# Performance work log

Measured on AMD Instinct MI355X. Metric: run time of the kernel, lower is better.

## Reference

```python
import jax, jax.numpy as jnp
import numpy as np

B, N, E, H = 8, 1024, 768, 12
HD = E // H

def setup_inputs() -> dict:
    key = jax.random.key(0)
    k1, k2, k3, k4, k5 = jax.random.split(key, 5)
    s = 0.02
    return {
        'query': jax.random.normal(k1, (B, N, E), dtype=jnp.float32),
        'qkv_w': jax.random.normal(k2, (3 * E, E), dtype=jnp.float32) * s,
        'qkv_b': jax.random.normal(k3, (3 * E,), dtype=jnp.float32) * s,
        'out_w': jax.random.normal(k4, (E, E), dtype=jnp.float32) * s,
        'out_b': jax.random.normal(k5, (E,), dtype=jnp.float32) * s,
    }

def reference(query, qkv_w, qkv_b, out_w, out_b):
    b, n, e = query.shape
    scale = HD ** -0.5
    # torch Linear: x @ W^T + b
    qkv = query @ qkv_w.T + qkv_b              # [B,N,3E]
    qkv = qkv.reshape(b, n, 3, H, HD)
    q = qkv[:, :, 0].transpose(0, 2, 1, 3)     # [B,H,N,hd]
    k = qkv[:, :, 1].transpose(0, 2, 1, 3)
    v = qkv[:, :, 2].transpose(0, 2, 1, 3)
    attn = jnp.einsum('bhqd,bhkd->bhqk', q, k) * scale
    attn = jax.nn.softmax(attn, axis=-1)
    x = jnp.einsum('bhqk,bhkd->bhqd', attn, v)  # [B,H,N,hd]
    x = x.transpose(0, 2, 1, 3).reshape(b, n, e)
    return x @ out_w.T + out_b
```

## Files before the change

### kernel.cpp

```cpp
#include <hip/hip_runtime.h>
#include <cstdint>
#include <cstddef>

#define QSCALE 0.18033688011112042f

typedef __bf16 bf16x8 __attribute__((ext_vector_type(8)));
typedef __bf16 bf16x4 __attribute__((ext_vector_type(4)));
typedef short short4v __attribute__((ext_vector_type(4)));
typedef float floatx4 __attribute__((ext_vector_type(4)));

static __device__ __forceinline__ uint16_t f2bf(float f) {
    uint32_t u = __builtin_bit_cast(uint32_t, f);
    u += 0x7FFFu + ((u >> 16) & 1u);
    return (uint16_t)(u >> 16);
}

static __device__ __forceinline__ void st_bf16(uint16_t* p, float f) {
    *(__bf16*)p = (__bf16)f;
}

static __device__ __forceinline__ bf16x8 ld_frag(const uint16_t* p) {
    uint4 u = *(const uint4*)p;
    return __builtin_bit_cast(bf16x8, u);
}

static __device__ __forceinline__ void async_lds16(const uint16_t* g, uint16_t* l) {
    __builtin_amdgcn_global_load_lds(
        (const __attribute__((address_space(1))) void*)g,
        (__attribute__((address_space(3))) void*)l,
        16, 0, 0);
}

static __device__ __forceinline__ size_t qk_swz(int bh, int idx, int hd) {
    return (size_t)bh * 65536 + (size_t)(idx >> 4) * 1024 + (size_t)(hd >> 5) * 512
         + (size_t)((hd & 31) >> 3) * 128 + (size_t)(idx & 15) * 8 + (hd & 7);
}
static __device__ __forceinline__ size_t v_swz(int bh, int hd, int key) {
    return (size_t)bh * 65536 + (size_t)(key >> 6) * 4096 + (size_t)(hd >> 4) * 1024
         + (size_t)((key >> 4) & 3) * 256 + (size_t)((key >> 2) & 3) * 64
         + (size_t)(hd & 15) * 4 + (key & 3);
}

__global__ __launch_bounds__(256) void cast3_kernel(
    const float* __restrict__ a, uint16_t* __restrict__ da, int na8,
    const float* __restrict__ b, uint16_t* __restrict__ db, int nb8,
    const float* __restrict__ c, uint16_t* __restrict__ dc, int nc8)
{
    int i = blockIdx.x * 256 + threadIdx.x;
    const float* src; uint16_t* dst; int idx;
    if (i < na8)                { src = a; dst = da; idx = i; }
    else if (i < na8 + nb8)     { src = b; dst = db; idx = i - na8; }
    else if (i < na8 + nb8 + nc8){ src = c; dst = dc; idx = i - na8 - nb8; }
    else return;
    const float4* p = (const float4*)src + (size_t)2 * idx;
    float4 x = p[0], y = p[1];
    uint32_t w0 = (uint32_t)f2bf(x.x) | ((uint32_t)f2bf(x.y) << 16);
    uint32_t w1 = (uint32_t)f2bf(x.z) | ((uint32_t)f2bf(x.w) << 16);
    uint32_t w2 = (uint32_t)f2bf(y.x) | ((uint32_t)f2bf(y.y) << 16);
    uint32_t w3 = (uint32_t)f2bf(y.z) | ((uint32_t)f2bf(y.w) << 16);
    uint4 v; v.x = w0; v.y = w1; v.z = w2; v.w = w3;
    *((uint4*)dst + idx) = v;
}

__global__ __launch_bounds__(256) void gemm_qkv_kernel(
    const uint16_t* __restrict__ X,
    const uint16_t* __restrict__ W,
    const float* __restrict__ bias,
    uint16_t* __restrict__ Qs, uint16_t* __restrict__ Ks, uint16_t* __restrict__ Vs)
{
    __shared__ __align__(16) uint16_t As[128 * 32];
    __shared__ __align__(16) uint16_t Bs[128 * 32];
    const int tid = threadIdx.x;
    const int wave = tid >> 6, lane = tid & 63;
    const int L = lane & 15, quad = lane >> 4;
    const int wM = (wave >> 1) * 64, wN = (wave & 1) * 64;
    const int bm = blockIdx.x * 128;
    const int bn = blockIdx.y * 128;

    floatx4 zero4 = {0.f, 0.f, 0.f, 0.f};
    floatx4 acc[4][4];
    #pragma unroll
    for (int i = 0; i < 4; ++i)
        #pragma unroll
        for (int j = 0; j < 4; ++j) acc[i][j] = zero4;

    const int srow = tid >> 2;
    const int scol = ((tid & 3) ^ ((srow >> 1) & 3)) * 8;
    const uint16_t* xp0 = X + (size_t)(bm + srow) * 768 + scol;
    const uint16_t* xp1 = xp0 + (size_t)64 * 768;
    const uint16_t* wp0 = W + (size_t)(bn + srow) * 768 + scol;
    const uint16_t* wp1 = wp0 + (size_t)64 * 768;
    uint16_t* lA0 = As + wave * 512;
    uint16_t* lA1 = As + 2048 + wave * 512;
    uint16_t* lB0 = Bs + wave * 512;
    uint16_t* lB1 = Bs + 2048 + wave * 512;

    const int cq = (quad ^ ((L >> 1) & 3)) * 8;

    for (int k0 = 0; k0 < 768; k0 += 32) {
        __syncthreads();
        async_lds16(xp0 + k0, lA0);
        async_lds16(xp1 + k0, lA1);
        async_lds16(wp0 + k0, lB0);
        async_lds16(wp1 + k0, lB1);
        __syncthreads();
        bf16x8 af[4], bfr[4];
        #pragma unroll
        for (int mi = 0; mi < 4; ++mi) af[mi]  = ld_frag(&As[(wM + mi * 16 + L) * 32 + cq]);
        #pragma unroll
        for (int ni = 0; ni < 4; ++ni) bfr[ni] = ld_frag(&Bs[(wN + ni * 16 + L) * 32 + cq]);
        #pragma unroll
        for (int mi = 0; mi < 4; ++mi)
            #pragma unroll
            for (int ni = 0; ni < 4; ++ni)
                acc[mi][ni] = __builtin_amdgcn_mfma_f32_16x16x32_bf16(
                    af[mi], bfr[ni], acc[mi][ni], 0, 0, 0);
    }

    const int part = bn / 768;
    #pragma unroll
    for (int ni = 0; ni < 4; ++ni) {
        int col = bn + wN + ni * 16 + L;
        int c = col - part * 768;
        int h = c >> 6, hd = c & 63;
        float bv = bias[col];
        #pragma unroll
        for (int mi = 0; mi < 4; ++mi) {
            #pragma unroll
            for (int r = 0; r < 4; ++r) {
                int m = bm + wM + mi * 16 + quad * 4 + r;
                int b = m >> 10, ns = m & 1023;
                int bh = b * 12 + h;
                float v = acc[mi][ni][r] + bv;
                if (part == 0)      st_bf16(&Qs[qk_swz(bh, ns, hd)], v * QSCALE);
                else if (part == 1) st_bf16(&Ks[qk_swz(bh, ns, hd)], v);
                else                st_bf16(&Vs[v_swz(bh, hd, ns)], v);
            }
        }
    }
}

__global__ __launch_bounds__(256) void attn_kernel(
    const uint16_t* __restrict__ Qs,
    const uint16_t* __restrict__ Ks,
    const uint16_t* __restrict__ Vs,
    uint16_t* __restrict__ Ob)
{
    const int tid = threadIdx.x;
    const int wave = tid >> 6, lane = tid & 63;
    const int L = lane & 15, quad = lane >> 4;
    const int bh = blockIdx.x;
    const int qt = blockIdx.y;
    const int b = bh / 12, h = bh - b * 12;
    const int q0 = qt * 128 + wave * 32;

    floatx4 zero4 = {0.f, 0.f, 0.f, 0.f};

    const uint16_t* qbase = Qs + (size_t)bh * 65536 + (size_t)lane * 8;
    bf16x8 aq[2][2];
    #pragma unroll
    for (int st = 0; st < 2; ++st) {
        const uint16_t* qp = qbase + (size_t)(qt * 8 + wave * 2 + st) * 1024;
        aq[st][0] = ld_frag(qp);
        aq[st][1] = ld_frag(qp + 512);
    }

    floatx4 accO[2][4];
    #pragma unroll
    for (int st = 0; st < 2; ++st)
        #pragma unroll
        for (int t = 0; t < 4; ++t) accO[st][t] = zero4;
    float lacc[2] = {0.f, 0.f};

    const uint16_t* kbase = Ks + (size_t)bh * 65536 + (size_t)lane * 8;
    const uint16_t* vbase = Vs + (size_t)bh * 65536 + (size_t)lane * 4;

    for (int j = 0; j < 16; ++j) {
        bf16x8 ka[4][2];
        #pragma unroll
        for (int kc = 0; kc < 4; ++kc) {
            const uint16_t* kp = kbase + (size_t)(j * 4 + kc) * 1024;
            ka[kc][0] = ld_frag(kp);
            ka[kc][1] = ld_frag(kp + 512);
        }
        short4v va[4][4];
        const uint16_t* vp = vbase + (size_t)j * 4096;
        #pragma unroll
        for (int t = 0; t < 4; ++t)
            #pragma unroll
            for (int kc = 0; kc < 4; ++kc)
                va[kc][t] = *(const short4v*)(vp + t * 1024 + kc * 256);

        floatx4 c[2][4];
        #pragma unroll
        for (int st = 0; st < 2; ++st)
            #pragma unroll
            for (int kc = 0; kc < 4; ++kc) {
                floatx4 z = zero4;
                z = __builtin_amdgcn_mfma_f32_16x16x32_bf16(ka[kc][0], aq[st][0], z, 0, 0, 0);
                z = __builtin_amdgcn_mfma_f32_16x16x32_bf16(ka[kc][1], aq[st][1], z, 0, 0, 0);
                c[st][kc] = z;
            }

        short4v pb[2][4];
        #pragma unroll
        for (int st = 0; st < 2; ++st)
            #pragma unroll
            for (int kc = 0; kc < 4; ++kc) {
                float p0 = __builtin_amdgcn_exp2f(c[st][kc][0]);
                float p1 = __builtin_amdgcn_exp2f(c[st][kc][1]);
                float p2 = __builtin_amdgcn_exp2f(c[st][kc][2]);
                float p3 = __builtin_amdgcn_exp2f(c[st][kc][3]);
                lacc[st] += (p0 + p1) + (p2 + p3);
                bf16x4 t4;
                t4.x = (__bf16)p0; t4.y = (__bf16)p1;
                t4.z = (__bf16)p2; t4.w = (__bf16)p3;
                pb[st][kc] = __builtin_bit_cast(short4v, t4);
            }

        #pragma unroll
        for (int st = 0; st < 2; ++st)
            #pragma unroll
            for (int t = 0; t < 4; ++t)
                #pragma unroll
                for (int kc = 0; kc < 4; ++kc)
                    accO[st][t] = __builtin_amdgcn_mfma_f32_16x16x16bf16_1k(
                        va[kc][t], pb[st][kc], accO[st][t], 0, 0, 0);
    }

    #pragma unroll
    for (int st = 0; st < 2; ++st) {
        float sum = lacc[st];
        sum += __shfl_xor(sum, 16);
        sum += __shfl_xor(sum, 32);
        float inv = 1.f / sum;
        uint16_t* orow = Ob + ((size_t)b * 1024 + q0 + st * 16 + L) * 768 + h * 64 + quad * 4;
        #pragma unroll
        for (int t = 0; t < 4; ++t) {
            bf16x4 o4;
            o4.x = (__bf16)(accO[st][t][0] * inv);
            o4.y = (__bf16)(accO[st][t][1] * inv);
            o4.z = (__bf16)(accO[st][t][2] * inv);
            o4.w = (__bf16)(accO[st][t][3] * inv);
            *(uint2*)(orow + t * 16) = __builtin_bit_cast(uint2, o4);
        }
    }
}

__global__ __launch_bounds__(256) void gemm_out_kernel(
    const uint16_t* __restrict__ X,
    const uint16_t* __restrict__ W,
    const float* __restrict__ bias,
    float* __restrict__ out)
{
    __shared__ __align__(16) uint16_t As[128 * 32];
    __shared__ __align__(16) uint16_t Bs[64 * 32];
    const int tid = threadIdx.x;
    const int wave = tid >> 6, lane = tid & 63;
    const int L = lane & 15, quad = lane >> 4;
    const int wM = (wave >> 1) * 64, wN = (wave & 1) * 32;
    const int bm = blockIdx.x * 128;
    const int bn = blockIdx.y * 64;

    floatx4 zero4 = {0.f, 0.f, 0.f, 0.f};
    floatx4 acc[4][2];
    #pragma unroll
    for (int i = 0; i < 4; ++i)
        #pragma unroll
        for (int j = 0; j < 2; ++j) acc[i][j] = zero4;

    const int srow = tid >> 2;
    const int scol = ((tid & 3) ^ ((srow >> 1) & 3)) * 8;
    const uint16_t* xp0 = X + (size_t)(bm + srow) * 768 + scol;
    const uint16_t* xp1 = xp0 + (size_t)64 * 768;
    const uint16_t* wp0 = W + (size_t)(bn + srow) * 768 + scol;
    uint16_t* lA0 = As + wave * 512;
    uint16_t* lA1 = As + 2048 + wave * 512;
    uint16_t* lB0 = Bs + wave * 512;

    const int cq = (quad ^ ((L >> 1) & 3)) * 8;

    for (int k0 = 0; k0 < 768; k0 += 32) {
        __syncthreads();
        async_lds16(xp0 + k0, lA0);
        async_lds16(xp1 + k0, lA1);
        async_lds16(wp0 + k0, lB0);
        __syncthreads();
        bf16x8 af[4], bfr[2];
        #pragma unroll
        for (int mi = 0; mi < 4; ++mi) af[mi]  = ld_frag(&As[(wM + mi * 16 + L) * 32 + cq]);
        #pragma unroll
        for (int ni = 0; ni < 2; ++ni) bfr[ni] = ld_frag(&Bs[(wN + ni * 16 + L) * 32 + cq]);
        #pragma unroll
        for (int mi = 0; mi < 4; ++mi)
            #pragma unroll
            for (int ni = 0; ni < 2; ++ni)
                acc[mi][ni] = __builtin_amdgcn_mfma_f32_16x16x32_bf16(
                    af[mi], bfr[ni], acc[mi][ni], 0, 0, 0);
    }

    #pragma unroll
    for (int ni = 0; ni < 2; ++ni) {
        int col = bn + wN + ni * 16 + L;
        float bv = bias[col];
        #pragma unroll
        for (int mi = 0; mi < 4; ++mi)
            #pragma unroll
            for (int r = 0; r < 4; ++r) {
                int m = bm + wM + mi * 16 + quad * 4 + r;
                out[(size_t)m * 768 + col] = acc[mi][ni][r] + bv;
            }
    }
}

extern "C" void kernel_launch(void* const* d_in, const int* in_sizes, int n_in,
                              void* d_out, int out_size, void* d_ws, size_t ws_size,
                              hipStream_t stream) {
    const float* query = (const float*)d_in[0];
    const float* qkv_w = (const float*)d_in[1];
    const float* qkv_b = (const float*)d_in[2];
    const float* out_w = (const float*)d_in[3];
    const float* out_b = (const float*)d_in[4];
    float* out = (float*)d_out;

    uint8_t* ws = (uint8_t*)d_ws;
    uint16_t* Xb  = (uint16_t*)(ws);
    uint16_t* W1b = (uint16_t*)(ws + 12582912);
    uint16_t* W2b = (uint16_t*)(ws + 16121856);
    uint16_t* Qsw = (uint16_t*)(ws + 17301504);
    uint16_t* Ksw = (uint16_t*)(ws + 29884416);
    uint16_t* Vsw = (uint16_t*)(ws + 42467328);
    uint16_t* Ab  = Xb;

    cast3_kernel<<<4224, 256, 0, stream>>>(query, Xb, 786432,
                                           qkv_w, W1b, 221184,
                                           out_w, W2b, 73728);
    gemm_qkv_kernel<<<dim3(64, 18), 256, 0, stream>>>(Xb, W1b, qkv_b, Qsw, Ksw, Vsw);
    attn_kernel<<<dim3(96, 8), 256, 0, stream>>>(Qsw, Ksw, Vsw, Ab);
    gemm_out_kernel<<<dim3(64, 12), 256, 0, stream>>>(Ab, W2b, out_b, out);
}
```

Baseline: 191.8 us.

## Double-buffer LDS tiles in QKV and output GEMM kernels

Both GEMM kernels now keep two LDS buffers for the A and B tiles. The next K-slice is issued to the spare buffer with async global-to-LDS loads before the current slice's MFMAs run. This leaves one barrier per iteration instead of two, and lets global-load latency overlap with matrix math. In exchange, shared memory per block doubles, which may reduce occupancy. The overlap may also be partly lost if the barrier forces a full wait on outstanding vector memory operations.

```diff
diff --git a/kernel.cpp b/kernel.cpp
--- a/kernel.cpp
+++ b/kernel.cpp
@@ -68,8 +68,8 @@
     const float* __restrict__ bias,
     uint16_t* __restrict__ Qs, uint16_t* __restrict__ Ks, uint16_t* __restrict__ Vs)
 {
-    __shared__ __align__(16) uint16_t As[128 * 32];
-    __shared__ __align__(16) uint16_t Bs[128 * 32];
+    __shared__ __align__(16) uint16_t As[2][128 * 32];
+    __shared__ __align__(16) uint16_t Bs[2][128 * 32];
     const int tid = threadIdx.x;
     const int wave = tid >> 6, lane = tid & 63;
     const int L = lane & 15, quad = lane >> 4;
@@ -90,31 +90,39 @@
     const uint16_t* xp1 = xp0 + (size_t)64 * 768;
     const uint16_t* wp0 = W + (size_t)(bn + srow) * 768 + scol;
     const uint16_t* wp1 = wp0 + (size_t)64 * 768;
-    uint16_t* lA0 = As + wave * 512;
-    uint16_t* lA1 = As + 2048 + wave * 512;
-    uint16_t* lB0 = Bs + wave * 512;
-    uint16_t* lB1 = Bs + 2048 + wave * 512;
+    const int lofs = wave * 512;
 
     const int cq = (quad ^ ((L >> 1) & 3)) * 8;
 
+    async_lds16(xp0, &As[0][lofs]);
+    async_lds16(xp1, &As[0][2048 + lofs]);
+    async_lds16(wp0, &Bs[0][lofs]);
+    async_lds16(wp1, &Bs[0][2048 + lofs]);
+    __syncthreads();
+
+    int cur = 0;
     for (int k0 = 0; k0 < 768; k0 += 32) {
-        __syncthreads();
-        async_lds16(xp0 + k0, lA0);
-        async_lds16(xp1 + k0, lA1);
-        async_lds16(wp0 + k0, lB0);
-        async_lds16(wp1 + k0, lB1);
-        __syncthreads();
+        const int kn = k0 + 32;
+        if (kn < 768) {
+            const int nxt = cur ^ 1;
+            async_lds16(xp0 + kn, &As[nxt][lofs]);
+            async_lds16(xp1 + kn, &As[nxt][2048 + lofs]);
+            async_lds16(wp0 + kn, &Bs[nxt][lofs]);
+            async_lds16(wp1 + kn, &Bs[nxt][2048 + lofs]);
+        }
         bf16x8 af[4], bfr[4];
         #pragma unroll
-        for (int mi = 0; mi < 4; ++mi) af[mi]  = ld_frag(&As[(wM + mi * 16 + L) * 32 + cq]);
-        #pragma unroll
-        for (int ni = 0; ni < 4; ++ni) bfr[ni] = ld_frag(&Bs[(wN + ni * 16 + L) * 32 + cq]);
+        for (int mi = 0; mi < 4; ++mi) af[mi]  = ld_frag(&As[cur][(wM + mi * 16 + L) * 32 + cq]);
+        #pragma unroll
+        for (int ni = 0; ni < 4; ++ni) bfr[ni] = ld_frag(&Bs[cur][(wN + ni * 16 + L) * 32 + cq]);
         #pragma unroll
         for (int mi = 0; mi < 4; ++mi)
             #pragma unroll
             for (int ni = 0; ni < 4; ++ni)
                 acc[mi][ni] = __builtin_amdgcn_mfma_f32_16x16x32_bf16(
                     af[mi], bfr[ni], acc[mi][ni], 0, 0, 0);
+        __syncthreads();
+        cur ^= 1;
     }
 
     const int part = bn / 768;
@@ -253,8 +261,8 @@
     const float* __restrict__ bias,
     float* __restrict__ out)
 {
-    __shared__ __align__(16) uint16_t As[128 * 32];
-    __shared__ __align__(16) uint16_t Bs[64 * 32];
+    __shared__ __align__(16) uint16_t As[2][128 * 32];
+    __shared__ __align__(16) uint16_t Bs[2][64 * 32];
     const int tid = threadIdx.x;
     const int wave = tid >> 6, lane = tid & 63;
     const int L = lane & 15, quad = lane >> 4;
@@ -274,29 +282,37 @@
     const uint16_t* xp0 = X + (size_t)(bm + srow) * 768 + scol;
     const uint16_t* xp1 = xp0 + (size_t)64 * 768;
     const uint16_t* wp0 = W + (size_t)(bn + srow) * 768 + scol;
-    uint16_t* lA0 = As + wave * 512;
-    uint16_t* lA1 = As + 2048 + wave * 512;
-    uint16_t* lB0 = Bs + wave * 512;
+    const int lofs = wave * 512;
 
     const int cq = (quad ^ ((L >> 1) & 3)) * 8;
 
+    async_lds16(xp0, &As[0][lofs]);
+    async_lds16(xp1, &As[0][2048 + lofs]);
+    async_lds16(wp0, &Bs[0][lofs]);
+    __syncthreads();
+
+    int cur = 0;
     for (int k0 = 0; k0 < 768; k0 += 32) {
-        __syncthreads();
-        async_lds16(xp0 + k0, lA0);
-        async_lds16(xp1 + k0, lA1);
-        async_lds16(wp0 + k0, lB0);
-        __syncthreads();
+        const int kn = k0 + 32;
+        if (kn < 768) {
+            const int nxt = cur ^ 1;
+            async_lds16(xp0 + kn, &As[nxt][lofs]);
+            async_lds16(xp1 + kn, &As[nxt][2048 + lofs]);
+            async_lds16(wp0 + kn, &Bs[nxt][lofs]);
+        }
         bf16x8 af[4], bfr[2];
         #pragma unroll
-        for (int mi = 0; mi < 4; ++mi) af[mi]  = ld_frag(&As[(wM + mi * 16 + L) * 32 + cq]);
-        #pragma unroll
-        for (int ni = 0; ni < 2; ++ni) bfr[ni] = ld_frag(&Bs[(wN + ni * 16 + L) * 32 + cq]);
+        for (int mi = 0; mi < 4; ++mi) af[mi]  = ld_frag(&As[cur][(wM + mi * 16 + L) * 32 + cq]);
+        #pragma unroll
+        for (int ni = 0; ni < 2; ++ni) bfr[ni] = ld_frag(&Bs[cur][(wN + ni * 16 + L) * 32 + cq]);
         #pragma unroll
         for (int mi = 0; mi < 4; ++mi)
             #pragma unroll
             for (int ni = 0; ni < 2; ++ni)
                 acc[mi][ni] = __builtin_amdgcn_mfma_f32_16x16x32_bf16(
                     af[mi], bfr[ni], acc[mi][ni], 0, 0, 0);
+        __syncthreads();
+        cur ^= 1;
     }
 
     #pragma unroll
```

New measurement: 198.1 us. 3.3% more time.

## Triple-buffer LDS tiles in QKV and output GEMMs with async prefetch two stages ahead

Applied to the files above, without the earlier changes.

Both projection GEMMs now keep three LDS buffers and issue direct-to-LDS global loads two k-steps ahead. Explicit vmcnt waits and a single barrier per iteration replace the two __syncthreads that used to surround each load. The goal is to hide global memory latency behind MFMA work, at the cost of three times the LDS footprint, which may reduce occupancy. Correctness now depends on vmcnt counting only the async loads.

```diff
diff --git a/kernel.cpp b/kernel.cpp
--- a/kernel.cpp
+++ b/kernel.cpp
@@ -8,6 +8,10 @@
 typedef __bf16 bf16x4 __attribute__((ext_vector_type(4)));
 typedef short short4v __attribute__((ext_vector_type(4)));
 typedef float floatx4 __attribute__((ext_vector_type(4)));
+
+#define WAITVM4() asm volatile("s_waitcnt vmcnt(4)" ::: "memory")
+#define WAITVM3() asm volatile("s_waitcnt vmcnt(3)" ::: "memory")
+#define WAITVM0() asm volatile("s_waitcnt vmcnt(0)" ::: "memory")
 
 static __device__ __forceinline__ uint16_t f2bf(float f) {
     uint32_t u = __builtin_bit_cast(uint32_t, f);
@@ -62,14 +66,31 @@
     *((uint4*)dst + idx) = v;
 }
 
+static __device__ __forceinline__ void qkv_step(
+    const uint16_t* Abuf, const uint16_t* Bbuf,
+    int wM, int wN, int L, int cq, floatx4 acc[4][4])
+{
+    bf16x8 af[4], bfr[4];
+    #pragma unroll
+    for (int mi = 0; mi < 4; ++mi) af[mi]  = ld_frag(&Abuf[(wM + mi * 16 + L) * 32 + cq]);
+    #pragma unroll
+    for (int ni = 0; ni < 4; ++ni) bfr[ni] = ld_frag(&Bbuf[(wN + ni * 16 + L) * 32 + cq]);
+    #pragma unroll
+    for (int mi = 0; mi < 4; ++mi)
+        #pragma unroll
+        for (int ni = 0; ni < 4; ++ni)
+            acc[mi][ni] = __builtin_amdgcn_mfma_f32_16x16x32_bf16(
+                af[mi], bfr[ni], acc[mi][ni], 0, 0, 0);
+}
+
 __global__ __launch_bounds__(256) void gemm_qkv_kernel(
     const uint16_t* __restrict__ X,
     const uint16_t* __restrict__ W,
     const float* __restrict__ bias,
     uint16_t* __restrict__ Qs, uint16_t* __restrict__ Ks, uint16_t* __restrict__ Vs)
 {
-    __shared__ __align__(16) uint16_t As[128 * 32];
-    __shared__ __align__(16) uint16_t Bs[128 * 32];
+    __shared__ __align__(16) uint16_t As[3][128 * 32];
+    __shared__ __align__(16) uint16_t Bs[3][128 * 32];
     const int tid = threadIdx.x;
     const int wave = tid >> 6, lane = tid & 63;
     const int L = lane & 15, quad = lane >> 4;
@@ -90,32 +111,40 @@
     const uint16_t* xp1 = xp0 + (size_t)64 * 768;
     const uint16_t* wp0 = W + (size_t)(bn + srow) * 768 + scol;
     const uint16_t* wp1 = wp0 + (size_t)64 * 768;
-    uint16_t* lA0 = As + wave * 512;
-    uint16_t* lA1 = As + 2048 + wave * 512;
-    uint16_t* lB0 = Bs + wave * 512;
-    uint16_t* lB1 = Bs + 2048 + wave * 512;
+    const int lofs = wave * 512;
 
     const int cq = (quad ^ ((L >> 1) & 3)) * 8;
 
-    for (int k0 = 0; k0 < 768; k0 += 32) {
-        __syncthreads();
-        async_lds16(xp0 + k0, lA0);
-        async_lds16(xp1 + k0, lA1);
-        async_lds16(wp0 + k0, lB0);
-        async_lds16(wp1 + k0, lB1);
-        __syncthreads();
-        bf16x8 af[4], bfr[4];
-        #pragma unroll
-        for (int mi = 0; mi < 4; ++mi) af[mi]  = ld_frag(&As[(wM + mi * 16 + L) * 32 + cq]);
-        #pragma unroll
-        for (int ni = 0; ni < 4; ++ni) bfr[ni] = ld_frag(&Bs[(wN + ni * 16 + L) * 32 + cq]);
-        #pragma unroll
-        for (int mi = 0; mi < 4; ++mi)
-            #pragma unroll
-            for (int ni = 0; ni < 4; ++ni)
-                acc[mi][ni] = __builtin_amdgcn_mfma_f32_16x16x32_bf16(
-                    af[mi], bfr[ni], acc[mi][ni], 0, 0, 0);
-    }
+    uint16_t* aR = As[0]; uint16_t* aN = As[1]; uint16_t* aW = As[2];
+    uint16_t* bR = Bs[0]; uint16_t* bN = Bs[1]; uint16_t* bW = Bs[2];
+
+    async_lds16(xp0,      aR + lofs);
+    async_lds16(xp1,      aR + 2048 + lofs);
+    async_lds16(wp0,      bR + lofs);
+    async_lds16(wp1,      bR + 2048 + lofs);
+    async_lds16(xp0 + 32, aN + lofs);
+    async_lds16(xp1 + 32, aN + 2048 + lofs);
+    async_lds16(wp0 + 32, bN + lofs);
+    async_lds16(wp1 + 32, bN + 2048 + lofs);
+    WAITVM4();
+    __builtin_amdgcn_s_barrier();
+
+    for (int t = 0; t < 22; ++t) {
+        const int kf = t * 32 + 64;
+        async_lds16(xp0 + kf, aW + lofs);
+        async_lds16(xp1 + kf, aW + 2048 + lofs);
+        async_lds16(wp0 + kf, bW + lofs);
+        async_lds16(wp1 + kf, bW + 2048 + lofs);
+        qkv_step(aR, bR, wM, wN, L, cq, acc);
+        WAITVM4();
+        __builtin_amdgcn_s_barrier();
+        uint16_t* ta = aR; aR = aN; aN = aW; aW = ta;
+        uint16_t* tb = bR; bR = bN; bN = bW; bW = tb;
+    }
+    qkv_step(aR, bR, wM, wN, L, cq, acc);
+    WAITVM0();
+    __builtin_amdgcn_s_barrier();
+    qkv_step(aN, bN, wM, wN, L, cq, acc);
 
     const int part = bn / 768;
     #pragma unroll
@@ -247,14 +276,31 @@
     }
 }
 
+static __device__ __forceinline__ void out_step(
+    const uint16_t* Abuf, const uint16_t* Bbuf,
+    int wM, int wN, int L, int cq, floatx4 acc[4][2])
+{
+    bf16x8 af[4], bfr[2];
+    #pragma unroll
+    for (int mi = 0; mi < 4; ++mi) af[mi]  = ld_frag(&Abuf[(wM + mi * 16 + L) * 32 + cq]);
+    #pragma unroll
+    for (int ni = 0; ni < 2; ++ni) bfr[ni] = ld_frag(&Bbuf[(wN + ni * 16 + L) * 32 + cq]);
+    #pragma unroll
+    for (int mi = 0; mi < 4; ++mi)
+        #pragma unroll
+        for (int ni = 0; ni < 2; ++ni)
+            acc[mi][ni] = __builtin_amdgcn_mfma_f32_16x16x32_bf16(
+                af[mi], bfr[ni], acc[mi][ni], 0, 0, 0);
+}
+
 __global__ __launch_bounds__(256) void gemm_out_kernel(
     const uint16_t* __restrict__ X,
     const uint16_t* __restrict__ W,
     const float* __restrict__ bias,
     float* __restrict__ out)
 {
-    __shared__ __align__(16) uint16_t As[128 * 32];
-    __shared__ __align__(16) uint16_t Bs[64 * 32];
+    __shared__ __align__(16) uint16_t As[3][128 * 32];
+    __shared__ __align__(16) uint16_t Bs[3][64 * 32];
     const int tid = threadIdx.x;
     const int wave = tid >> 6, lane = tid & 63;
     const int L = lane & 15, quad = lane >> 4;
@@ -274,30 +320,37 @@
     const uint16_t* xp0 = X + (size_t)(bm + srow) * 768 + scol;
     const uint16_t* xp1 = xp0 + (size_t)64 * 768;
     const uint16_t* wp0 = W + (size_t)(bn + srow) * 768 + scol;
-    uint16_t* lA0 = As + wave * 512;
-    uint16_t* lA1 = As + 2048 + wave * 512;
-    uint16_t* lB0 = Bs + wave * 512;
+    const int lofs = wave * 512;
 
     const int cq = (quad ^ ((L >> 1) & 3)) * 8;
 
-    for (int k0 = 0; k0 < 768; k0 += 32) {
-        __syncthreads();
-        async_lds16(xp0 + k0, lA0);
-        async_lds16(xp1 + k0, lA1);
-        async_lds16(wp0 + k0, lB0);
-        __syncthreads();
-        bf16x8 af[4], bfr[2];
-        #pragma unroll
-        for (int mi = 0; mi < 4; ++mi) af[mi]  = ld_frag(&As[(wM + mi * 16 + L) * 32 + cq]);
-        #pragma unroll
-        for (int ni = 0; ni < 2; ++ni) bfr[ni] = ld_frag(&Bs[(wN + ni * 16 + L) * 32 + cq]);
-        #pragma unroll
-        for (int mi = 0; mi < 4; ++mi)
-            #pragma unroll
-            for (int ni = 0; ni < 2; ++ni)
-                acc[mi][ni] = __builtin_amdgcn_mfma_f32_16x16x32_bf16(
-                    af[mi], bfr[ni], acc[mi][ni], 0, 0, 0);
-    }
+    uint16_t* aR = As[0]; uint16_t* aN = As[1]; uint16_t* aW = As[2];
+    uint16_t* bR = Bs[0]; uint16_t* bN = Bs[1]; uint16_t* bW = Bs[2];
+
+    async_lds16(xp0,      aR + lofs);
+    async_lds16(xp1,      aR + 2048 + lofs);
+    async_lds16(wp0,      bR + lofs);
+    async_lds16(xp0 + 32, aN + lofs);
+    async_lds16(xp1 + 32, aN + 2048 + lofs);
+    async_lds16(wp0 + 32, bN + lofs);
+    WAITVM3();
+    __builtin_amdgcn_s_barrier();
+
+    for (int t = 0; t < 22; ++t) {
+        const int kf = t * 32 + 64;
+        async_lds16(xp0 + kf, aW + lofs);
+        async_lds16(xp1 + kf, aW + 2048 + lofs);
+        async_lds16(wp0 + kf, bW + lofs);
+        out_step(aR, bR, wM, wN, L, cq, acc);
+        WAITVM3();
+        __builtin_amdgcn_s_barrier();
+        uint16_t* ta = aR; aR = aN; aN = aW; aW = ta;
+        uint16_t* tb = bR; bR = bN; bN = bW; bW = tb;
+    }
+    out_step(aR, bR, wM, wN, L, cq, acc);
+    WAITVM0();
+    __builtin_amdgcn_s_barrier();
+    out_step(aN, bN, wM, wN, L, cq, acc);
 
     #pragma unroll
     for (int ni = 0; ni < 2; ++ni) {
```

New measurement: 207.2 us. 1.08x slower.

## Pre-swizzle X and W into MFMA fragment layout, load QKV GEMM operands directly

Applied to the files above, without the earlier changes.

The cast kernel now writes X and the QKV weight in a fragment-major layout, where each 16-row by 32-k tile is laid out so a lane's 8 bf16 values are contiguous. The QKV GEMM drops its LDS staging and barriers and loads operand fragments straight from global memory into registers, double-buffered across k-steps. The aim is to remove LDS traffic and syncthreads from the GEMM. In exchange each wave re-reads operands from global or L2 with no sharing across waves, and the cast kernel's reads become strided.

```diff
diff --git a/kernel.cpp b/kernel.cpp
--- a/kernel.cpp
+++ b/kernel.cpp
@@ -47,12 +47,20 @@
     const float* __restrict__ c, uint16_t* __restrict__ dc, int nc8)
 {
     int i = blockIdx.x * 256 + threadIdx.x;
-    const float* src; uint16_t* dst; int idx;
-    if (i < na8)                { src = a; dst = da; idx = i; }
-    else if (i < na8 + nb8)     { src = b; dst = db; idx = i - na8; }
-    else if (i < na8 + nb8 + nc8){ src = c; dst = dc; idx = i - na8 - nb8; }
+    const float* src; uint16_t* dst; int idx; int swz;
+    if (i < na8)                { src = a; dst = da; idx = i; swz = 1; }
+    else if (i < na8 + nb8)     { src = b; dst = db; idx = i - na8; swz = 1; }
+    else if (i < na8 + nb8 + nc8){ src = c; dst = dc; idx = i - na8 - nb8; swz = 0; }
     else return;
-    const float4* p = (const float4*)src + (size_t)2 * idx;
+    size_t srcElem;
+    if (swz) {
+        int frag = idx >> 6, ln = idx & 63;
+        int m16 = frag / 24, kt = frag - m16 * 24;
+        srcElem = (size_t)(m16 * 16 + (ln & 15)) * 768 + kt * 32 + (ln >> 4) * 8;
+    } else {
+        srcElem = (size_t)idx * 8;
+    }
+    const float4* p = (const float4*)(src + srcElem);
     float4 x = p[0], y = p[1];
     uint32_t w0 = (uint32_t)f2bf(x.x) | ((uint32_t)f2bf(x.y) << 16);
     uint32_t w1 = (uint32_t)f2bf(x.z) | ((uint32_t)f2bf(x.w) << 16);
@@ -68,8 +76,6 @@
     const float* __restrict__ bias,
     uint16_t* __restrict__ Qs, uint16_t* __restrict__ Ks, uint16_t* __restrict__ Vs)
 {
-    __shared__ __align__(16) uint16_t As[128 * 32];
-    __shared__ __align__(16) uint16_t Bs[128 * 32];
     const int tid = threadIdx.x;
     const int wave = tid >> 6, lane = tid & 63;
     const int L = lane & 15, quad = lane >> 4;
@@ -84,37 +90,38 @@
         #pragma unroll
         for (int j = 0; j < 4; ++j) acc[i][j] = zero4;
 
-    const int srow = tid >> 2;
-    const int scol = ((tid & 3) ^ ((srow >> 1) & 3)) * 8;
-    const uint16_t* xp0 = X + (size_t)(bm + srow) * 768 + scol;
-    const uint16_t* xp1 = xp0 + (size_t)64 * 768;
-    const uint16_t* wp0 = W + (size_t)(bn + srow) * 768 + scol;
-    const uint16_t* wp1 = wp0 + (size_t)64 * 768;
-    uint16_t* lA0 = As + wave * 512;
-    uint16_t* lA1 = As + 2048 + wave * 512;
-    uint16_t* lB0 = Bs + wave * 512;
-    uint16_t* lB1 = Bs + 2048 + wave * 512;
-
-    const int cq = (quad ^ ((L >> 1) & 3)) * 8;
-
-    for (int k0 = 0; k0 < 768; k0 += 32) {
-        __syncthreads();
-        async_lds16(xp0 + k0, lA0);
-        async_lds16(xp1 + k0, lA1);
-        async_lds16(wp0 + k0, lB0);
-        async_lds16(wp1 + k0, lB1);
-        __syncthreads();
-        bf16x8 af[4], bfr[4];
-        #pragma unroll
-        for (int mi = 0; mi < 4; ++mi) af[mi]  = ld_frag(&As[(wM + mi * 16 + L) * 32 + cq]);
-        #pragma unroll
-        for (int ni = 0; ni < 4; ++ni) bfr[ni] = ld_frag(&Bs[(wN + ni * 16 + L) * 32 + cq]);
+    const uint16_t* ab = X + (size_t)((bm + wM) >> 4) * 24 * 512 + (size_t)lane * 8;
+    const uint16_t* bb = W + (size_t)((bn + wN) >> 4) * 24 * 512 + (size_t)lane * 8;
+
+    bf16x8 a0[4], b0[4], a1[4], b1[4];
+    #pragma unroll
+    for (int mi = 0; mi < 4; ++mi) a0[mi] = ld_frag(ab + (size_t)(mi * 24 + 0) * 512);
+    #pragma unroll
+    for (int ni = 0; ni < 4; ++ni) b0[ni] = ld_frag(bb + (size_t)(ni * 24 + 0) * 512);
+
+    for (int t = 0; t < 24; t += 2) {
+        #pragma unroll
+        for (int mi = 0; mi < 4; ++mi) a1[mi] = ld_frag(ab + (size_t)(mi * 24 + t + 1) * 512);
+        #pragma unroll
+        for (int ni = 0; ni < 4; ++ni) b1[ni] = ld_frag(bb + (size_t)(ni * 24 + t + 1) * 512);
         #pragma unroll
         for (int mi = 0; mi < 4; ++mi)
             #pragma unroll
             for (int ni = 0; ni < 4; ++ni)
                 acc[mi][ni] = __builtin_amdgcn_mfma_f32_16x16x32_bf16(
-                    af[mi], bfr[ni], acc[mi][ni], 0, 0, 0);
+                    a0[mi], b0[ni], acc[mi][ni], 0, 0, 0);
+        if (t + 2 < 24) {
+            #pragma unroll
+            for (int mi = 0; mi < 4; ++mi) a0[mi] = ld_frag(ab + (size_t)(mi * 24 + t + 2) * 512);
+            #pragma unroll
+            for (int ni = 0; ni < 4; ++ni) b0[ni] = ld_frag(bb + (size_t)(ni * 24 + t + 2) * 512);
+        }
+        #pragma unroll
+        for (int mi = 0; mi < 4; ++mi)
+            #pragma unroll
+            for (int ni = 0; ni < 4; ++ni)
+                acc[mi][ni] = __builtin_amdgcn_mfma_f32_16x16x32_bf16(
+                    a1[mi], b1[ni], acc[mi][ni], 0, 0, 0);
     }
 
     const int part = bn / 768;
```

Result: slower. 201.0 us (+4.8%).
